# Kernel optimization log

Hardware: AMD Instinct MI355X
Metric: run time of the kernel (lower is better)

## Reference

```python
import jax, jax.numpy as jnp
import numpy as np

FP, ENC, H, OUT, STEPS = 4860, 512, 512, 42, 128


def _lin(k, fan_in, fan_out, scale=0.02):
    kw, kb = jax.random.split(k)
    W = jax.random.normal(kw, (fan_out, fan_in), jnp.float32) * scale
    b = jax.random.normal(kb, (fan_out,), jnp.float32) * scale
    return W, b


def setup_inputs() -> dict:
    key = jax.random.key(0)
    ks = jax.random.split(key, 12)
    x = jax.random.normal(ks[0], (2048, FP), jnp.float32)
    y = jax.random.normal(ks[1], (2048, STEPS, OUT), jnp.float32)
    eps = jax.random.normal(ks[2], (2048, ENC), jnp.float32)
    We1, be1 = _lin(ks[3], FP, 2048)
    We2, be2 = _lin(ks[4], 2048, 1024)
    We3, be3 = _lin(ks[5], 1024, 512)
    We41, be41 = _lin(ks[6], 512, ENC)
    Wih, bih = _lin(ks[7], ENC, 3 * H)    # GRU input weights [3H, ENC]
    Whh, bhh = _lin(ks[8], H, 3 * H)      # GRU hidden weights [3H, H]
    Wf1, bf1 = _lin(ks[9], H, OUT)        # EncoderDecoder.fc1
    Wf2, bf2 = _lin(ks[10], OUT, H)       # EncoderDecoder.fc2
    return dict(x=x, y=y, eps=eps,
                We1=We1, be1=be1, We2=We2, be2=be2, We3=We3, be3=be3,
                We41=We41, be41=be41,
                Wih=Wih, bih=bih, Whh=Whh, bhh=bhh,
                Wf1=Wf1, bf1=bf1, Wf2=Wf2, bf2=bf2,
                teacher_forcing=0)


def _forward(x, eps, We1, be1, We2, be2, We3, be3, We41, be41,
             Wih, bih, Whh, bhh, Wf1, bf1, Wf2, bf2):
    # VAE encoder (note: source uses fc41 for BOTH mu and logvar)
    h1 = jax.nn.relu(x @ We1.T + be1)
    h2 = jax.nn.relu(h1 @ We2.T + be2)
    h3 = jax.nn.relu(h2 @ We3.T + be3)
    mu = h3 @ We41.T + be41
    logvar = mu
    encoded = eps * jnp.exp(0.5 * logvar) + mu  # reparameterize, [B, ENC]

    B = x.shape[0]
    h0 = jnp.zeros((B, H), x.dtype)

    def step(carry, _):
        h, xt = carry                      # h: [B,H], xt: [B,ENC]
        gi = xt @ Wih.T + bih              # [B,3H]
        gh = h @ Whh.T + bhh               # [B,3H]
        r = jax.nn.sigmoid(gi[:, :H] + gh[:, :H])
        z = jax.nn.sigmoid(gi[:, H:2 * H] + gh[:, H:2 * H])
        n = jnp.tanh(gi[:, 2 * H:] + r * gh[:, 2 * H:])
        h_new = (1.0 - z) * n + z * h
        out = jax.nn.relu(h_new @ Wf1.T + bf1)   # [B,42]
        x_new = jax.nn.relu(out @ Wf2.T + bf2)   # [B,H] (no teacher forcing)
        return (h_new, x_new), out

    (_, _), outs = jax.lax.scan(step, (h0, encoded), None, length=STEPS)
    return jnp.transpose(outs, (1, 0, 2))  # [B, 128, 42]


def reference(x, y, eps, We1, be1, We2, be2, We3, be3, We41, be41,
              Wih, bih, Whh, bhh, Wf1, bf1, Wf2, bf2, teacher_forcing):
    # teacher_forcing=0 (False path); y unused in that branch.
    return _forward(x, eps, We1, be1, We2, be2, We3, be3, We41, be41,
                    Wih, bih, Whh, bhh, Wf1, bf1, Wf2, bf2)
```

## Files before the change

### kernel.cpp

```cpp
#include <hip/hip_runtime.h>
#include <hip/hip_bf16.h>
#include <cstdint>
#include <cstddef>

#define DEVI __device__ __forceinline__

typedef __attribute__((ext_vector_type(8))) short bf16x8;
typedef __attribute__((ext_vector_type(4))) float f32x4;
typedef unsigned short u16;
typedef unsigned int u32;
typedef unsigned long long u64;

DEVI u16 f2bf(float f) {
    u32 i = __builtin_bit_cast(u32, f);
    u32 r = (i + 0x7FFFu + ((i >> 16) & 1u)) >> 16;
    return (u16)r;
}
DEVI float sigmoidf_(float x) { return 1.0f / (1.0f + __expf(-x)); }
DEVI float tanhf_(float x) { return 2.0f / (1.0f + __expf(-2.0f * x)) - 1.0f; }

typedef const __attribute__((address_space(1))) void* gptr_t;
typedef __attribute__((address_space(3))) void* lptr_t;

DEVI void gload16(const void* g, void* l) {
    __builtin_amdgcn_global_load_lds((gptr_t)g, (lptr_t)l, 16, 0, 0);
}

__global__ void fill_const(float* __restrict__ p, int n, float v) {
    int i = blockIdx.x * 256 + threadIdx.x;
    if (i < n) p[i] = v;
}

__global__ void cvt_pad(const float* __restrict__ src, u16* __restrict__ dst,
                        int wcols, int cols, int spitch, int dpitch) {
    int c = blockIdx.x * 256 + threadIdx.x;
    int r = blockIdx.y;
    if (c >= wcols) return;
    float v = (c < cols) ? src[(size_t)r * spitch + c] : 0.0f;
    dst[(size_t)r * dpitch + c] = f2bf(v);
}

__global__ void prep_wf1(const float* __restrict__ Wf1, u16* __restrict__ Wf1p) {
    int r = blockIdx.x;
    int c = threadIdx.x;
    Wf1p[r * 512 + c] = (r < 42) ? f2bf(Wf1[(size_t)r * 512 + c]) : (u16)0;
}
__global__ void prep_wf2(const float* __restrict__ Wf2, u16* __restrict__ Wf2p) {
    int c = blockIdx.x;
    int k = threadIdx.x;
    Wf2p[c * 64 + k] = (k < 42) ? f2bf(Wf2[(size_t)c * 42 + k]) : (u16)0;
}

template <int EPI>
__global__ __launch_bounds__(256) void gemm_bt(
    const u16* __restrict__ A, int lda, const u16* __restrict__ B, int ldb,
    const float* __restrict__ bias, u16* __restrict__ C, int ldc, int ktiles,
    const float* __restrict__ eps) {
    __shared__ u16 As[128 * 64];
    __shared__ u16 Bs[128 * 64];
    const int tid = threadIdx.x;
    const int lane = tid & 63;
    const int wave = tid >> 6;
    const int m0 = blockIdx.y * 128;
    const int n0 = blockIdx.x * 128;
    const int l15 = lane & 15, lg = lane >> 4;
    const int wm = (wave >> 1) * 64, wn = (wave & 1) * 64;

    f32x4 acc[4][4];
#pragma unroll
    for (int r = 0; r < 4; r++)
#pragma unroll
        for (int c = 0; c < 4; c++) acc[r][c] = (f32x4){0.f, 0.f, 0.f, 0.f};

    for (int t = 0; t < ktiles; ++t) {
        const int k0 = t * 64;
#pragma unroll
        for (int q = 0; q < 4; ++q) {
            int chunk = q * 4 + wave;
            int o = chunk * 1024 + lane * 16;
            int row = o >> 7;
            int cb = o & 127;
            gload16((const char*)(A + (size_t)(m0 + row) * lda + k0) + cb,
                    (char*)As + chunk * 1024);
            gload16((const char*)(B + (size_t)(n0 + row) * ldb + k0) + cb,
                    (char*)Bs + chunk * 1024);
        }
        __syncthreads();
#pragma unroll
        for (int kf = 0; kf < 2; ++kf) {
            bf16x8 a[4], b[4];
#pragma unroll
            for (int r = 0; r < 4; r++)
                a[r] = *(const bf16x8*)&As[(wm + 16 * r + l15) * 64 + kf * 32 + lg * 8];
#pragma unroll
            for (int c = 0; c < 4; c++)
                b[c] = *(const bf16x8*)&Bs[(wn + 16 * c + l15) * 64 + kf * 32 + lg * 8];
#pragma unroll
            for (int r = 0; r < 4; r++)
#pragma unroll
                for (int c = 0; c < 4; c++)
                    acc[r][c] = __builtin_amdgcn_mfma_f32_16x16x32_bf16(
                        a[r], b[c], acc[r][c], 0, 0, 0);
        }
        __syncthreads();
    }
#pragma unroll
    for (int r = 0; r < 4; r++) {
#pragma unroll
        for (int c = 0; c < 4; c++) {
            int col = n0 + wn + 16 * c + l15;
            float bv = bias[col];
#pragma unroll
            for (int i = 0; i < 4; i++) {
                int row = m0 + wm + 16 * r + lg * 4 + i;
                float v = acc[r][c][i] + bv;
                if (EPI == 0) {
                    v = v > 0.f ? v : 0.f;
                    C[(size_t)row * ldc + col] = f2bf(v);
                } else {
                    float e = eps[(size_t)row * 512 + col];
                    float enc = e * __expf(0.5f * v) + v;
                    C[(size_t)row * ldc + col] = f2bf(enc);
                }
            }
        }
    }
}

template <int MODE>
__global__ __launch_bounds__(1024, 1) void gru_step(
    const u16* __restrict__ xt0, const u16* __restrict__ hbR,
    const float* __restrict__ hfR, u16* __restrict__ hbW,
    float* __restrict__ hfW, const u16* __restrict__ WB,
    const float* __restrict__ bih, const float* __restrict__ bhh,
    const u16* __restrict__ Wf1p, const float* __restrict__ bf1,
    const u16* __restrict__ Wf2p, const float* __restrict__ bf2,
    float* __restrict__ outp, int sidx) {
    __shared__ __align__(16) u16 xtL[64 * 512];
    __shared__ __align__(16) u16 Bst[2][192 * 64];
    __shared__ __align__(16) u16 oL[64 * 64];
    const int tid = threadIdx.x, lane = tid & 63, wave = tid >> 6;
    const int wr = wave >> 2, wu = wave & 3;
    const int l15 = lane & 15, lg = lane >> 4;
    const int bid = blockIdx.x;
    const int sb = (MODE == 2) ? 0 : (bid & 7);
    const int rb = (MODE == 2) ? bid : (bid >> 3);
    const int S = sb * 64, m0 = rb * 64;

    if (MODE == 0) {
#pragma unroll
        for (int k2 = 0; k2 < 4; ++k2) {
            int j = tid + k2 * 1024;
            int row = j >> 6, slot = j & 63;
            gload16((const char*)(xt0 + (size_t)(m0 + row) * 512) + (slot ^ (row & 7)) * 16,
                    (char*)xtL + j * 16);
        }
    }

    if (MODE >= 1) {
        if (MODE == 1) {
            ((u64*)oL)[tid] = 0ull;
            __syncthreads();
        }
        if (wu < 3) {
            f32x4 oa = (f32x4){0.f, 0.f, 0.f, 0.f};
            const u16* ha = hbR + (size_t)(m0 + 16 * wr + l15) * 512 + lg * 8;
            const u16* wb1 = Wf1p + (size_t)(16 * wu + l15) * 512 + lg * 8;
#pragma unroll
            for (int kf = 0; kf < 16; ++kf) {
                bf16x8 a = *(const bf16x8*)(ha + kf * 32);
                bf16x8 b = *(const bf16x8*)(wb1 + kf * 32);
                oa = __builtin_amdgcn_mfma_f32_16x16x32_bf16(a, b, oa, 0, 0, 0);
            }
            int col = 16 * wu + l15;
            float bv = (col < 42) ? bf1[col] : 0.f;
#pragma unroll
            for (int i = 0; i < 4; ++i) {
                int row = 16 * wr + lg * 4 + i;
                float v = oa[i] + bv;
                v = v > 0.f ? v : 0.f;
                if (MODE == 1) {
                    int cb = col * 2;
                    *(u16*)((char*)oL + row * 128 +
                            (((cb & ~15) ^ ((row & 7) << 4)) | (cb & 15))) = f2bf(v);
                }
                if (sb == 0 && col < 42)
                    outp[(size_t)(m0 + row) * 5376 + (size_t)sidx * 42 + col] = v;
            }
        }
    }

    if (MODE == 1) {
        __syncthreads();
        bf16x8 a2[2];
#pragma unroll
        for (int kf = 0; kf < 2; ++kf) {
            int row = 16 * wr + l15;
            a2[kf] = *(const bf16x8*)((char*)oL + row * 128 +
                                      ((kf * 64 + lg * 16) ^ ((row & 7) << 4)));
        }
#pragma unroll
        for (int ci = 0; ci < 8; ++ci) {
            int col = 128 * wu + 16 * ci + l15;
            const u16* wb2 = Wf2p + (size_t)col * 64 + lg * 8;
            f32x4 xa = (f32x4){0.f, 0.f, 0.f, 0.f};
            xa = __builtin_amdgcn_mfma_f32_16x16x32_bf16(a2[0], *(const bf16x8*)wb2, xa, 0, 0, 0);
            xa = __builtin_amdgcn_mfma_f32_16x16x32_bf16(a2[1], *(const bf16x8*)(wb2 + 32), xa, 0, 0, 0);
            float bv = bf2[col];
            int cb = col * 2;
#pragma unroll
            for (int i = 0; i < 4; ++i) {
                int row = 16 * wr + lg * 4 + i;
                float v = xa[i] + bv;
                v = v > 0.f ? v : 0.f;
                *(u16*)((char*)xtL + row * 1024 +
                        (((cb & ~15) ^ ((row & 7) << 4)) | (cb & 15))) = f2bf(v);
            }
        }
    }

    if (MODE <= 1) {
        auto stageB = [&](int buf, int t) {
            {
                int j = tid;
                int row = j >> 3, slot = j & 7;
                int gate = row >> 6, unit = row & 63;
                gload16(WB + (size_t)(gate * 512 + S + unit) * 1024 + t * 64 +
                            (slot ^ (row & 7)) * 8,
                        (char*)Bst + buf * 24576 + j * 16);
            }
            if (tid < 512) {
                int j = tid + 1024;
                int row = j >> 3, slot = j & 7;
                int gate = row >> 6, unit = row & 63;
                gload16(WB + (size_t)(gate * 512 + S + unit) * 1024 + t * 64 +
                            (slot ^ (row & 7)) * 8,
                        (char*)Bst + buf * 24576 + j * 16);
            }
        };
        f32x4 ar = (f32x4){0.f, 0.f, 0.f, 0.f};
        f32x4 az = ar, agi = ar, agh = ar;
        const u16* hrow = hbR + (size_t)(m0 + 16 * wr + l15) * 512 + lg * 8;
        bf16x8 hc0, hc1, hp0, hp1;

        stageB(0, 0);
        __syncthreads();

        for (int t = 0; t < 16; ++t) {
            if (t >= 7 && t < 15) {
                const u16* hs = hrow + (t + 1 - 8) * 64;
                hp0 = *(const bf16x8*)hs;
                hp1 = *(const bf16x8*)(hs + 32);
            }
            if (t < 15) stageB((t + 1) & 1, t + 1);

            bf16x8 a[2];
            if (t < 8) {
                int row = 16 * wr + l15;
#pragma unroll
                for (int kf = 0; kf < 2; ++kf)
                    a[kf] = *(const bf16x8*)((char*)xtL + row * 1024 +
                                             ((t * 128 + kf * 64 + lg * 16) ^ ((row & 7) << 4)));
            } else {
                a[0] = hc0;
                a[1] = hc1;
            }
            const char* bb = (const char*)Bst + (t & 1) * 24576;
            int rb0 = 16 * wu + l15;
            int sw = (rb0 & 7) << 4;
#pragma unroll
            for (int kf = 0; kf < 2; ++kf) {
                int kb = kf * 64 + lg * 16;
                bf16x8 br = *(const bf16x8*)(bb + (size_t)rb0 * 128 + (kb ^ sw));
                bf16x8 bz = *(const bf16x8*)(bb + (size_t)(64 + rb0) * 128 + (kb ^ sw));
                bf16x8 bn = *(const bf16x8*)(bb + (size_t)(128 + rb0) * 128 + (kb ^ sw));
                ar = __builtin_amdgcn_mfma_f32_16x16x32_bf16(a[kf], br, ar, 0, 0, 0);
                az = __builtin_amdgcn_mfma_f32_16x16x32_bf16(a[kf], bz, az, 0, 0, 0);
                if (t < 8)
                    agi = __builtin_amdgcn_mfma_f32_16x16x32_bf16(a[kf], bn, agi, 0, 0, 0);
                else
                    agh = __builtin_amdgcn_mfma_f32_16x16x32_bf16(a[kf], bn, agh, 0, 0, 0);
            }
            hc0 = hp0;
            hc1 = hp1;
            __syncthreads();
        }
        int hu = S + 16 * wu + l15;
        float br_ = bih[hu] + bhh[hu];
        float bz_ = bih[512 + hu] + bhh[512 + hu];
        float bgi = bih[1024 + hu];
        float bgh = bhh[1024 + hu];
#pragma unroll
        for (int i = 0; i < 4; ++i) {
            int row = m0 + 16 * wr + lg * 4 + i;
            float rv = sigmoidf_(ar[i] + br_);
            float zv = sigmoidf_(az[i] + bz_);
            float nv = tanhf_(agi[i] + bgi + rv * (agh[i] + bgh));
            float hold = hfR[(size_t)row * 512 + hu];
            float hn = (1.f - zv) * nv + zv * hold;
            hfW[(size_t)row * 512 + hu] = hn;
            hbW[(size_t)row * 512 + hu] = f2bf(hn);
        }
    }
}

extern "C" void kernel_launch(void* const* d_in, const int* in_sizes, int n_in,
                              void* d_out, int out_size, void* d_ws,
                              size_t ws_size, hipStream_t stream) {
    (void)in_sizes; (void)n_in; (void)out_size;
    const float* x = (const float*)d_in[0];
    const float* eps = (const float*)d_in[2];
    const float* We1 = (const float*)d_in[3];
    const float* be1 = (const float*)d_in[4];
    const float* We2 = (const float*)d_in[5];
    const float* be2 = (const float*)d_in[6];
    const float* We3 = (const float*)d_in[7];
    const float* be3 = (const float*)d_in[8];
    const float* We41 = (const float*)d_in[9];
    const float* be41 = (const float*)d_in[10];
    const float* Wih = (const float*)d_in[11];
    const float* bih = (const float*)d_in[12];
    const float* Whh = (const float*)d_in[13];
    const float* bhh = (const float*)d_in[14];
    const float* Wf1 = (const float*)d_in[15];
    const float* bf1 = (const float*)d_in[16];
    const float* Wf2 = (const float*)d_in[17];
    const float* bf2 = (const float*)d_in[18];
    float* out = (float*)d_out;

    char* ws = (char*)d_ws;
    size_t off = 0;
    auto alloc = [&](size_t bytes) -> char* {
        char* p = ws + off;
        off += (bytes + 255) & ~(size_t)255;
        return p;
    };
    u16* xb = (u16*)alloc(2048ull * 4864 * 2);
    u16* We1b = (u16*)alloc(2048ull * 4864 * 2);
    u16* We2b = (u16*)alloc(1024ull * 2048 * 2);
    u16* We3b = (u16*)alloc(512ull * 1024 * 2);
    u16* We41b = (u16*)alloc(512ull * 512 * 2);
    u16* WB = (u16*)alloc(1536ull * 1024 * 2);
    u16* h1b = (u16*)alloc(2048ull * 2048 * 2);
    u16* h2b = (u16*)alloc(2048ull * 1024 * 2);
    u16* h3b = (u16*)alloc(2048ull * 512 * 2);
    u16* encb = (u16*)alloc(2048ull * 512 * 2);
    u16* hb0 = (u16*)alloc(2048ull * 512 * 2);
    u16* hb1 = (u16*)alloc(2048ull * 512 * 2);
    float* hf0 = (float*)alloc(2048ull * 512 * 4);
    float* hf1 = (float*)alloc(2048ull * 512 * 4);
    u16* Wf1p = (u16*)alloc(48ull * 512 * 2);
    u16* Wf2p = (u16*)alloc(512ull * 64 * 2);
    if (off > ws_size) {
        fill_const<<<(11010048 + 255) / 256, 256, 0, stream>>>(out, 11010048, 54321.0f);
        return;
    }
    u16* hb[2] = {hb0, hb1};
    float* hfl[2] = {hf0, hf1};

    auto cdiv = [](int a, int b) { return (a + b - 1) / b; };
    cvt_pad<<<dim3(cdiv(4864, 256), 2048), 256, 0, stream>>>(x, xb, 4864, 4860, 4860, 4864);
    cvt_pad<<<dim3(cdiv(4864, 256), 2048), 256, 0, stream>>>(We1, We1b, 4864, 4860, 4860, 4864);
    cvt_pad<<<dim3(cdiv(2048, 256), 1024), 256, 0, stream>>>(We2, We2b, 2048, 2048, 2048, 2048);
    cvt_pad<<<dim3(cdiv(1024, 256), 512), 256, 0, stream>>>(We3, We3b, 1024, 1024, 1024, 1024);
    cvt_pad<<<dim3(cdiv(512, 256), 512), 256, 0, stream>>>(We41, We41b, 512, 512, 512, 512);
    cvt_pad<<<dim3(cdiv(512, 256), 1536), 256, 0, stream>>>(Wih, WB, 512, 512, 512, 1024);
    cvt_pad<<<dim3(cdiv(512, 256), 1536), 256, 0, stream>>>(Whh, WB + 512, 512, 512, 512, 1024);
    prep_wf1<<<48, 512, 0, stream>>>(Wf1, Wf1p);
    prep_wf2<<<512, 64, 0, stream>>>(Wf2, Wf2p);
    hipMemsetAsync(hb0, 0, 2048ull * 512 * 2, stream);
    hipMemsetAsync(hf0, 0, 2048ull * 512 * 4, stream);

    gemm_bt<0><<<dim3(16, 16), 256, 0, stream>>>(xb, 4864, We1b, 4864, be1, h1b, 2048, 76, nullptr);
    gemm_bt<0><<<dim3(8, 16), 256, 0, stream>>>(h1b, 2048, We2b, 2048, be2, h2b, 1024, 32, nullptr);
    gemm_bt<0><<<dim3(4, 16), 256, 0, stream>>>(h2b, 1024, We3b, 1024, be3, h3b, 512, 16, nullptr);
    gemm_bt<1><<<dim3(4, 16), 256, 0, stream>>>(h3b, 512, We41b, 512, be41, encb, 512, 8, eps);

    gru_step<0><<<256, 1024, 0, stream>>>(encb, hb0, hf0, hb1, hf1, WB, bih,
                                          bhh, Wf1p, bf1, Wf2p, bf2, out, 0);
    for (int i = 1; i < 128; ++i) {
        int p = i & 1;
        gru_step<1><<<256, 1024, 0, stream>>>(nullptr, hb[p], hfl[p],
                                              hb[p ^ 1], hfl[p ^ 1], WB, bih,
                                              bhh, Wf1p, bf1, Wf2p, bf2, out,
                                              i - 1);
    }
    gru_step<2><<<32, 1024, 0, stream>>>(nullptr, hb0, hf0, nullptr, nullptr,
                                         WB, bih, bhh, Wf1p, bf1, Wf2p, bf2,
                                         out, 127);
}
```

Baseline: 4.947 ms.

## Stream GRU weights directly from global into registers and fuse prep kernels

```diff
diff --git a/kernel.cpp b/kernel.cpp
--- a/kernel.cpp
+++ b/kernel.cpp
@@ -18,6 +18,7 @@
 }
 DEVI float sigmoidf_(float x) { return 1.0f / (1.0f + __expf(-x)); }
 DEVI float tanhf_(float x) { return 2.0f / (1.0f + __expf(-2.0f * x)) - 1.0f; }
+DEVI float reluf_(float x) { return x > 0.f ? x : 0.f; }
 
 typedef const __attribute__((address_space(1))) void* gptr_t;
 typedef __attribute__((address_space(3))) void* lptr_t;
@@ -31,24 +32,54 @@
     if (i < n) p[i] = v;
 }
 
-__global__ void cvt_pad(const float* __restrict__ src, u16* __restrict__ dst,
-                        int wcols, int cols, int spitch, int dpitch) {
-    int c = blockIdx.x * 256 + threadIdx.x;
-    int r = blockIdx.y;
-    if (c >= wcols) return;
-    float v = (c < cols) ? src[(size_t)r * spitch + c] : 0.0f;
-    dst[(size_t)r * dpitch + c] = f2bf(v);
-}
-
-__global__ void prep_wf1(const float* __restrict__ Wf1, u16* __restrict__ Wf1p) {
-    int r = blockIdx.x;
-    int c = threadIdx.x;
-    Wf1p[r * 512 + c] = (r < 42) ? f2bf(Wf1[(size_t)r * 512 + c]) : (u16)0;
-}
-__global__ void prep_wf2(const float* __restrict__ Wf2, u16* __restrict__ Wf2p) {
-    int c = blockIdx.x;
-    int k = threadIdx.x;
-    Wf2p[c * 64 + k] = (k < 42) ? f2bf(Wf2[(size_t)c * 42 + k]) : (u16)0;
+__global__ void prep_all(const float* __restrict__ x, const float* __restrict__ We1,
+                         const float* __restrict__ We2, const float* __restrict__ We3,
+                         const float* __restrict__ We41, const float* __restrict__ Wih,
+                         const float* __restrict__ Whh, const float* __restrict__ Wf1,
+                         const float* __restrict__ Wf2, u16* __restrict__ xb,
+                         u16* __restrict__ We1b, u16* __restrict__ We2b,
+                         u16* __restrict__ We3b, u16* __restrict__ We41b,
+                         u16* __restrict__ WB, u16* __restrict__ Wf1p,
+                         u16* __restrict__ Wf2p) {
+    const long long T0 = 9961472, T1 = 19922944, T2 = 22020096, T3 = 22544384,
+                    T4 = 22806528, T5 = 23592960, T6 = 24379392, T7 = 24403968,
+                    T8 = 24436736;
+    for (long long i = (long long)blockIdx.x * 256 + threadIdx.x; i < T8;
+         i += (long long)gridDim.x * 256) {
+        if (i < T1) {
+            long long j = (i < T0) ? i : i - T0;
+            int r = (int)(j / 4864);
+            int c = (int)(j - (long long)r * 4864);
+            const float* s = (i < T0) ? x : We1;
+            u16* d = (i < T0) ? xb : We1b;
+            d[j] = (c < 4860) ? f2bf(s[(size_t)r * 4860 + c]) : (u16)0;
+        } else if (i < T2) {
+            int j = (int)(i - T1);
+            We2b[j] = f2bf(We2[j]);
+        } else if (i < T3) {
+            int j = (int)(i - T2);
+            We3b[j] = f2bf(We3[j]);
+        } else if (i < T4) {
+            int j = (int)(i - T3);
+            We41b[j] = f2bf(We41[j]);
+        } else if (i < T5) {
+            int j = (int)(i - T4);
+            int g = j >> 9, k = j & 511;
+            WB[(size_t)g * 1024 + k] = f2bf(Wih[j]);
+        } else if (i < T6) {
+            int j = (int)(i - T5);
+            int g = j >> 9, k = j & 511;
+            WB[(size_t)g * 1024 + 512 + k] = f2bf(Whh[j]);
+        } else if (i < T7) {
+            int j = (int)(i - T6);
+            int r = j >> 9;
+            Wf1p[j] = (r < 42) ? f2bf(Wf1[j]) : (u16)0;
+        } else {
+            int j = (int)(i - T7);
+            int c = j >> 6, k = j & 63;
+            Wf2p[j] = (k < 42) ? f2bf(Wf2[(size_t)c * 42 + k]) : (u16)0;
+        }
+    }
 }
 
 template <int EPI>
@@ -128,7 +159,7 @@
 }
 
 template <int MODE>
-__global__ __launch_bounds__(1024, 1) void gru_step(
+__global__ __launch_bounds__(1024, 2) void gru_step(
     const u16* __restrict__ xt0, const u16* __restrict__ hbR,
     const float* __restrict__ hfR, u16* __restrict__ hbW,
     float* __restrict__ hfW, const u16* __restrict__ WB,
@@ -137,7 +168,6 @@
     const u16* __restrict__ Wf2p, const float* __restrict__ bf2,
     float* __restrict__ outp, int sidx) {
     __shared__ __align__(16) u16 xtL[64 * 512];
-    __shared__ __align__(16) u16 Bst[2][192 * 64];
     __shared__ __align__(16) u16 oL[64 * 64];
     const int tid = threadIdx.x, lane = tid & 63, wave = tid >> 6;
     const int wr = wave >> 2, wu = wave & 3;
@@ -146,6 +176,7 @@
     const int sb = (MODE == 2) ? 0 : (bid & 7);
     const int rb = (MODE == 2) ? bid : (bid >> 3);
     const int S = sb * 64, m0 = rb * 64;
+    const int sw = (l15 & 7) << 4;
 
     if (MODE == 0) {
 #pragma unroll
@@ -155,6 +186,7 @@
             gload16((const char*)(xt0 + (size_t)(m0 + row) * 512) + (slot ^ (row & 7)) * 16,
                     (char*)xtL + j * 16);
         }
+        __syncthreads();
     }
 
     if (MODE >= 1) {
@@ -177,8 +209,8 @@
 #pragma unroll
             for (int i = 0; i < 4; ++i) {
                 int row = 16 * wr + lg * 4 + i;
-                float v = oa[i] + bv;
-                v = v > 0.f ? v : 0.f;
+                float v = reluf_(oa[i] + bv);
+                if (col >= 42) v = 0.f;
                 if (MODE == 1) {
                     int cb = col * 2;
                     *(u16*)((char*)oL + row * 128 +
@@ -211,79 +243,47 @@
 #pragma unroll
             for (int i = 0; i < 4; ++i) {
                 int row = 16 * wr + lg * 4 + i;
-                float v = xa[i] + bv;
-                v = v > 0.f ? v : 0.f;
+                float v = reluf_(xa[i] + bv);
                 *(u16*)((char*)xtL + row * 1024 +
                         (((cb & ~15) ^ ((row & 7) << 4)) | (cb & 15))) = f2bf(v);
             }
         }
+        __syncthreads();
     }
 
     if (MODE <= 1) {
-        auto stageB = [&](int buf, int t) {
-            {
-                int j = tid;
-                int row = j >> 3, slot = j & 7;
-                int gate = row >> 6, unit = row & 63;
-                gload16(WB + (size_t)(gate * 512 + S + unit) * 1024 + t * 64 +
-                            (slot ^ (row & 7)) * 8,
-                        (char*)Bst + buf * 24576 + j * 16);
-            }
-            if (tid < 512) {
-                int j = tid + 1024;
-                int row = j >> 3, slot = j & 7;
-                int gate = row >> 6, unit = row & 63;
-                gload16(WB + (size_t)(gate * 512 + S + unit) * 1024 + t * 64 +
-                            (slot ^ (row & 7)) * 8,
-                        (char*)Bst + buf * 24576 + j * 16);
-            }
-        };
         f32x4 ar = (f32x4){0.f, 0.f, 0.f, 0.f};
         f32x4 az = ar, agi = ar, agh = ar;
-        const u16* hrow = hbR + (size_t)(m0 + 16 * wr + l15) * 512 + lg * 8;
-        bf16x8 hc0, hc1, hp0, hp1;
-
-        stageB(0, 0);
-        __syncthreads();
-
-        for (int t = 0; t < 16; ++t) {
-            if (t >= 7 && t < 15) {
-                const u16* hs = hrow + (t + 1 - 8) * 64;
-                hp0 = *(const bf16x8*)hs;
-                hp1 = *(const bf16x8*)(hs + 32);
-            }
-            if (t < 15) stageB((t + 1) & 1, t + 1);
-
-            bf16x8 a[2];
-            if (t < 8) {
-                int row = 16 * wr + l15;
-#pragma unroll
-                for (int kf = 0; kf < 2; ++kf)
-                    a[kf] = *(const bf16x8*)((char*)xtL + row * 1024 +
-                                             ((t * 128 + kf * 64 + lg * 16) ^ ((row & 7) << 4)));
-            } else {
-                a[0] = hc0;
-                a[1] = hc1;
-            }
-            const char* bb = (const char*)Bst + (t & 1) * 24576;
-            int rb0 = 16 * wu + l15;
-            int sw = (rb0 & 7) << 4;
-#pragma unroll
-            for (int kf = 0; kf < 2; ++kf) {
-                int kb = kf * 64 + lg * 16;
-                bf16x8 br = *(const bf16x8*)(bb + (size_t)rb0 * 128 + (kb ^ sw));
-                bf16x8 bz = *(const bf16x8*)(bb + (size_t)(64 + rb0) * 128 + (kb ^ sw));
-                bf16x8 bn = *(const bf16x8*)(bb + (size_t)(128 + rb0) * 128 + (kb ^ sw));
-                ar = __builtin_amdgcn_mfma_f32_16x16x32_bf16(a[kf], br, ar, 0, 0, 0);
-                az = __builtin_amdgcn_mfma_f32_16x16x32_bf16(a[kf], bz, az, 0, 0, 0);
-                if (t < 8)
-                    agi = __builtin_amdgcn_mfma_f32_16x16x32_bf16(a[kf], bn, agi, 0, 0, 0);
-                else
-                    agh = __builtin_amdgcn_mfma_f32_16x16x32_bf16(a[kf], bn, agh, 0, 0, 0);
-            }
-            hc0 = hp0;
-            hc1 = hp1;
-            __syncthreads();
+        const u16* bpr = WB + (size_t)(S + wu * 16 + l15) * 1024 + lg * 8;
+        const u16* bpz = bpr + 512 * 1024;
+        const u16* bpn = bpz + 512 * 1024;
+        const int arow = 16 * wr + l15;
+        const u16* hA = hbR + (size_t)(m0 + arow) * 512 + lg * 8;
+        bf16x8 brA = *(const bf16x8*)(bpr);
+        bf16x8 bzA = *(const bf16x8*)(bpz);
+        bf16x8 bnA = *(const bf16x8*)(bpn);
+        bf16x8 brB, bzB, bnB;
+#pragma unroll 4
+        for (int t = 0; t < 32; ++t) {
+            if (t < 31) {
+                brB = *(const bf16x8*)(bpr + (t + 1) * 32);
+                bzB = *(const bf16x8*)(bpz + (t + 1) * 32);
+                bnB = *(const bf16x8*)(bpn + (t + 1) * 32);
+            }
+            bf16x8 a;
+            if (t < 16)
+                a = *(const bf16x8*)((char*)xtL + arow * 1024 + ((t * 64 + lg * 16) ^ sw));
+            else
+                a = *(const bf16x8*)(hA + (t - 16) * 32);
+            ar = __builtin_amdgcn_mfma_f32_16x16x32_bf16(a, brA, ar, 0, 0, 0);
+            az = __builtin_amdgcn_mfma_f32_16x16x32_bf16(a, bzA, az, 0, 0, 0);
+            if (t < 16)
+                agi = __builtin_amdgcn_mfma_f32_16x16x32_bf16(a, bnA, agi, 0, 0, 0);
+            else
+                agh = __builtin_amdgcn_mfma_f32_16x16x32_bf16(a, bnA, agh, 0, 0, 0);
+            brA = brB;
+            bzA = bzB;
+            bnA = bnB;
         }
         int hu = S + 16 * wu + l15;
         float br_ = bih[hu] + bhh[hu];
@@ -358,16 +358,8 @@
     u16* hb[2] = {hb0, hb1};
     float* hfl[2] = {hf0, hf1};
 
-    auto cdiv = [](int a, int b) { return (a + b - 1) / b; };
-    cvt_pad<<<dim3(cdiv(4864, 256), 2048), 256, 0, stream>>>(x, xb, 4864, 4860, 4860, 4864);
-    cvt_pad<<<dim3(cdiv(4864, 256), 2048), 256, 0, stream>>>(We1, We1b, 4864, 4860, 4860, 4864);
-    cvt_pad<<<dim3(cdiv(2048, 256), 1024), 256, 0, stream>>>(We2, We2b, 2048, 2048, 2048, 2048);
-    cvt_pad<<<dim3(cdiv(1024, 256), 512), 256, 0, stream>>>(We3, We3b, 1024, 1024, 1024, 1024);
-    cvt_pad<<<dim3(cdiv(512, 256), 512), 256, 0, stream>>>(We41, We41b, 512, 512, 512, 512);
-    cvt_pad<<<dim3(cdiv(512, 256), 1536), 256, 0, stream>>>(Wih, WB, 512, 512, 512, 1024);
-    cvt_pad<<<dim3(cdiv(512, 256), 1536), 256, 0, stream>>>(Whh, WB + 512, 512, 512, 512, 1024);
-    prep_wf1<<<48, 512, 0, stream>>>(Wf1, Wf1p);
-    prep_wf2<<<512, 64, 0, stream>>>(Wf2, Wf2p);
+    prep_all<<<8192, 256, 0, stream>>>(x, We1, We2, We3, We41, Wih, Whh, Wf1, Wf2,
+                                       xb, We1b, We2b, We3b, We41b, WB, Wf1p, Wf2p);
     hipMemsetAsync(hb0, 0, 2048ull * 512 * 2, stream);
     hipMemsetAsync(hf0, 0, 2048ull * 512 * 4, stream);
 
```

Measured after the change: 9.491 ms. 91.8% more time.
